# Performance work log

Measured on AMD Instinct MI355X. Metric: run time of the kernel, lower is better.

Reference implementation:

```python
import jax, jax.numpy as jnp
import numpy as np

B, N, FIN, FOUT = 8, 4096, 64, 64
NEG_SLOPE = 0.01  # torch LeakyReLU default


def setup_inputs() -> dict:
    key = jax.random.key(0)
    k1, k2, k3, k4, k5 = jax.random.split(key, 5)
    inp = jax.random.normal(k1, (B, N, FIN), dtype=jnp.float32)
    adj = jax.random.randint(k2, (N, N), 0, 2, dtype=jnp.int32)
    W_w = jax.random.normal(k3, (FOUT, FIN), dtype=jnp.float32) * (1.0 / np.sqrt(FIN))
    W_b = jax.random.normal(k4, (FOUT,), dtype=jnp.float32) * 0.01
    a = jax.random.normal(k5, (2 * FOUT, N), dtype=jnp.float32) * (1.414 / np.sqrt(2 * FOUT + N))
    return {"inp": inp, "adj": adj, "W_w": W_w, "W_b": W_b, "a": a}


def reference(inp, adj, W_w, W_b, a):
    # h = W(inp); h[:, 0, :] = 0
    h = jnp.einsum('bnf,of->bno', inp, W_w) + W_b          # [B, N, F]
    h = h.at[:, 0, :].set(0.0)

    # Original loop: for i in 1..N-1:
    #   ac = a[:, i]  (shape [2F, 1])
    #   index = where(adj[1:, i] > 0)  -> 0-based, used to index h directly (bug preserved)
    #   s_i = h[:, i, :] @ ac[:F] + sum_j h[:, index, :] @ ac[F:]   (scalar per batch)
    #   attention[:, i, :] = s_i broadcast over all columns
    # Empty-index case equals the general case since an empty neighbor sum is 0.
    mask = (adj[1:, :] > 0).astype(h.dtype)                # [N-1, N]
    neigh = jnp.einsum('ji,bjf->bif', mask, h[:, :N - 1, :])  # [B, N, F]
    s = (jnp.einsum('bif,fi->bi', h, a[:FOUT]) +
         jnp.einsum('bif,fi->bi', neigh, a[FOUT:]))        # [B, N]
    s = s.at[:, 0].set(0.0)                                # attention row 0 stays zero

    # h_prime = attention @ h, with attention[b,i,j] = s[b,i] for all j
    hsum = h.sum(axis=1)                                   # [B, F]
    h_prime = s[:, :, None] * hsum[:, None, :]             # [B, N, F]
    return jnp.where(h_prime >= 0, h_prime, NEG_SLOPE * h_prime)
```

## Files before the change

### kernel.cpp

```cpp
#include <hip/hip_runtime.h>
#include <hip/hip_bf16.h>

#define NN 4096

typedef unsigned short u16;
typedef __attribute__((ext_vector_type(8))) short short8;
typedef __attribute__((ext_vector_type(4))) float f32x4;
typedef __attribute__((ext_vector_type(4))) unsigned short u16x4;
typedef __attribute__((ext_vector_type(8))) unsigned short u16x8;
typedef __attribute__((ext_vector_type(4))) int i32x4;

typedef const void __attribute__((address_space(1)))* gas_t;
typedef void __attribute__((address_space(3)))* las_t;

__device__ __forceinline__ u16 f2bf(float x) {
  unsigned u = __float_as_uint(x);
  return (u16)((u + 0x7FFFu + ((u >> 16) & 1)) >> 16);
}

__global__ __launch_bounds__(256) void k_maskT(const int* __restrict__ adj, u16* __restrict__ maskT) {
  __shared__ __align__(16) u16 tile[128 * 132];
  const int i0 = blockIdx.x * 128, j0 = blockIdx.y * 128;
  const int t = threadIdx.x;
  const int jr = t >> 5, ic = (t & 31) * 4;
#pragma unroll
  for (int pass = 0; pass < 16; ++pass) {
    const int jl = pass * 8 + jr;
    const int j = j0 + jl;
    u16 v0 = 0, v1 = 0, v2 = 0, v3 = 0;
    if (j < NN - 1) {
      i32x4 av = *reinterpret_cast<const i32x4*>(&adj[(size_t)(j + 1) * NN + i0 + ic]);
      v0 = av.x > 0 ? 0x3F80 : 0;
      v1 = av.y > 0 ? 0x3F80 : 0;
      v2 = av.z > 0 ? 0x3F80 : 0;
      v3 = av.w > 0 ? 0x3F80 : 0;
    }
    tile[(ic + 0) * 132 + jl] = v0;
    tile[(ic + 1) * 132 + jl] = v1;
    tile[(ic + 2) * 132 + jl] = v2;
    tile[(ic + 3) * 132 + jl] = v3;
  }
  __syncthreads();
  const int ir = t >> 5, jc = (t & 31) * 4;
#pragma unroll
  for (int pass = 0; pass < 16; ++pass) {
    const int il = pass * 8 + ir;
    u16x4 o = *reinterpret_cast<const u16x4*>(&tile[il * 132 + jc]);
    *reinterpret_cast<u16x4*>(&maskT[(size_t)(i0 + il) * NN + j0 + jc]) = o;
  }
}

__global__ __launch_bounds__(256) void k_h(const float* __restrict__ inp, const float* __restrict__ Ww,
                                           const float* __restrict__ Wb, float* __restrict__ h,
                                           u16* __restrict__ h2t, float* __restrict__ hsum) {
  __shared__ __align__(16) u16 lA[128 * 64];
  __shared__ __align__(16) u16 lW[64 * 64];
  const int t = threadIdx.x, lane = t & 63, w = t >> 6;
  const int bid = blockIdx.x;
  const int b = bid >> 5;
  const size_t row0 = (size_t)bid * 128;
  {
    const int o = t >> 2, k0 = (t & 3) * 16;
    const float* src = &Ww[o * 64 + k0];
    u16 tmp[16];
#pragma unroll
    for (int e = 0; e < 16; ++e) tmp[e] = f2bf(src[e]);
    const int swz = (o & 7) * 8;
#pragma unroll
    for (int v = 0; v < 2; ++v)
      *reinterpret_cast<u16x8*>(&lW[o * 64 + ((k0 + v * 8) ^ swz)]) = *reinterpret_cast<u16x8*>(&tmp[v * 8]);
  }
  {
    const int r = t >> 1, k0 = (t & 1) * 32;
    const float* src = &inp[(row0 + r) * 64 + k0];
    u16 tmp[32];
#pragma unroll
    for (int e = 0; e < 32; ++e) tmp[e] = f2bf(src[e]);
    const int swz = (r & 7) * 8;
#pragma unroll
    for (int v = 0; v < 4; ++v)
      *reinterpret_cast<u16x8*>(&lA[r * 64 + ((k0 + v * 8) ^ swz)]) = *reinterpret_cast<u16x8*>(&tmp[v * 8]);
  }
  __syncthreads();
  f32x4 acc[2][4] = {};
#pragma unroll
  for (int ks = 0; ks < 2; ++ks) {
    const int kk = ks * 32 + (lane >> 4) * 8;
    short8 af[2], bf[4];
#pragma unroll
    for (int m = 0; m < 2; ++m) {
      const int row = w * 32 + m * 16 + (lane & 15);
      af[m] = *reinterpret_cast<const short8*>(&lA[row * 64 + (kk ^ ((row & 7) * 8))]);
    }
#pragma unroll
    for (int n = 0; n < 4; ++n) {
      const int o = n * 16 + (lane & 15);
      bf[n] = *reinterpret_cast<const short8*>(&lW[o * 64 + (kk ^ ((o & 7) * 8))]);
    }
#pragma unroll
    for (int m = 0; m < 2; ++m)
#pragma unroll
      for (int n = 0; n < 4; ++n)
        acc[m][n] = __builtin_amdgcn_mfma_f32_16x16x32_bf16(af[m], bf[n], acc[m][n], 0, 0, 0);
  }
  const int f0 = lane & 15;
  const int rsub = (lane >> 4) * 4;
  float wb[4];
#pragma unroll
  for (int n = 0; n < 4; ++n) wb[n] = Wb[n * 16 + f0];
  const int nloc_base = (bid & 31) * 128;
  float ps[4] = {0.f, 0.f, 0.f, 0.f};
#pragma unroll
  for (int m = 0; m < 2; ++m) {
    const int rl = w * 32 + m * 16 + rsub;
#pragma unroll
    for (int n = 0; n < 4; ++n) {
      u16 hb[4];
#pragma unroll
      for (int r = 0; r < 4; ++r) {
        float v = acc[m][n][r] + wb[n];
        if (nloc_base + rl + r == 0) v = 0.f;
        h[(row0 + rl + r) * 64 + n * 16 + f0] = v;
        hb[r] = f2bf(v);
        ps[n] += v;
      }
      *reinterpret_cast<u16x4*>(&h2t[(size_t)(b * 64 + n * 16 + f0) * NN + nloc_base + rl]) =
          *reinterpret_cast<u16x4*>(&hb[0]);
    }
  }
#pragma unroll
  for (int n = 0; n < 4; ++n) {
    float v = ps[n];
    v += __shfl_xor(v, 16);
    v += __shfl_xor(v, 32);
    if (lane < 16) atomicAdd(&hsum[b * 64 + n * 16 + f0], v);
  }
}

__global__ __launch_bounds__(256, 2) void k_gemm(const u16* __restrict__ A, const u16* __restrict__ Bm,
                                                 const float* __restrict__ a, float* __restrict__ s) {
  __shared__ __align__(16) u16 lA0[128 * 64], lA1[128 * 64];
  __shared__ __align__(16) u16 lB0[128 * 64], lB1[128 * 64];
  const int sid = blockIdx.x;
  const int wgid = (sid & 7) * 64 + (sid >> 3);
  const int c0 = (wgid & 3) * 128;
  const int i0 = ((wgid >> 2) & 31) * 128;
  const int z = wgid >> 7;
  const int t = threadIdx.x, lane = t & 63, w = t >> 6;
  const int wr = w >> 1, wc = w & 1;

  const int srow = lane >> 3;
  const int sk = ((lane & 7) ^ srow) * 8;
  const size_t kbase = (size_t)z * 1024;
  const u16* gA = A + (size_t)(i0 + w * 32 + srow) * NN + kbase + sk;
  const u16* gB = Bm + (size_t)(c0 + w * 32 + srow) * NN + kbase + sk;

#define STAGE_K(dstA, dstB, kt)                                                              \
  do {                                                                                       \
    _Pragma("unroll") for (int c = 0; c < 4; ++c) {                                          \
      __builtin_amdgcn_global_load_lds((gas_t)(gA + (size_t)(8 * c) * NN + (kt)),            \
                                       (las_t)((dstA) + (w * 32 + 8 * c) * 128 + lane * 16), \
                                       16, 0, 0);                                            \
      __builtin_amdgcn_global_load_lds((gas_t)(gB + (size_t)(8 * c) * NN + (kt)),            \
                                       (las_t)((dstB) + (w * 32 + 8 * c) * 128 + lane * 16), \
                                       16, 0, 0);                                            \
    }                                                                                        \
  } while (0)

  f32x4 acc[4][4] = {};
  STAGE_K((char*)lA0, (char*)lB0, 0);
  __syncthreads();
#pragma unroll 1
  for (int it = 0; it < 16; ++it) {
    char* nA = (it & 1) ? (char*)lA0 : (char*)lA1;
    char* nB = (it & 1) ? (char*)lB0 : (char*)lB1;
    if (it < 15) STAGE_K(nA, nB, (it + 1) * 64);
    const u16* cA = (it & 1) ? lA1 : lA0;
    const u16* cB = (it & 1) ? lB1 : lB0;
#pragma unroll
    for (int ks = 0; ks < 2; ++ks) {
      const int kb = ks * 4 + (lane >> 4);
      short8 af[4], bfr[4];
#pragma unroll
      for (int m = 0; m < 4; ++m) {
        const int row = wr * 64 + m * 16 + (lane & 15);
        af[m] = *reinterpret_cast<const short8*>(&cA[row * 64 + ((kb ^ (row & 7)) * 8)]);
      }
#pragma unroll
      for (int n = 0; n < 4; ++n) {
        const int row = wc * 64 + n * 16 + (lane & 15);
        bfr[n] = *reinterpret_cast<const short8*>(&cB[row * 64 + ((kb ^ (row & 7)) * 8)]);
      }
#pragma unroll
      for (int m = 0; m < 4; ++m)
#pragma unroll
        for (int n = 0; n < 4; ++n)
          acc[m][n] = __builtin_amdgcn_mfma_f32_16x16x32_bf16(af[m], bfr[n], acc[m][n], 0, 0, 0);
    }
    __syncthreads();
  }
#undef STAGE_K
  const int b = (c0 >> 7) * 2 + wc;
  const int f0 = lane & 15, rsub = (lane >> 4) * 4;
  float pp[4][4];
#pragma unroll
  for (int m = 0; m < 4; ++m) {
    const int irow = i0 + wr * 64 + m * 16 + rsub;
#pragma unroll
    for (int r = 0; r < 4; ++r) pp[m][r] = 0.f;
#pragma unroll
    for (int n = 0; n < 4; ++n) {
      f32x4 a2v = *reinterpret_cast<const f32x4*>(&a[(size_t)(64 + n * 16 + f0) * NN + irow]);
#pragma unroll
      for (int r = 0; r < 4; ++r) pp[m][r] += acc[m][n][r] * a2v[r];
    }
  }
#pragma unroll
  for (int m = 0; m < 4; ++m)
#pragma unroll
    for (int r = 0; r < 4; ++r) {
      float v = pp[m][r];
      v += __shfl_xor(v, 1);
      v += __shfl_xor(v, 2);
      v += __shfl_xor(v, 4);
      v += __shfl_xor(v, 8);
      pp[m][r] = v;
    }
  if (f0 == 0) {
    const int irow = i0 + wr * 64 + rsub;
#pragma unroll
    for (int m = 0; m < 4; ++m)
#pragma unroll
      for (int r = 0; r < 4; ++r)
        atomicAdd(&s[(size_t)b * NN + irow + m * 16 + r], pp[m][r]);
  }
}

__global__ __launch_bounds__(256) void k_final(const float* __restrict__ h, const float* __restrict__ sg,
                                               const float* __restrict__ a, const float* __restrict__ hsum,
                                               float* __restrict__ out) {
  __shared__ float a1[64][65];
  __shared__ float hs[64], sv[64];
  const int b = blockIdx.x >> 6;
  const int i0 = (blockIdx.x & 63) * 64;
  const int t = threadIdx.x;
  {
    const int lr = t >> 6, li = t & 63;
#pragma unroll
    for (int rr = 0; rr < 64; rr += 4)
      a1[rr + lr][li] = a[(size_t)(rr + lr) * NN + i0 + li];
    if (t < 64) hs[t] = hsum[b * 64 + t];
  }
  __syncthreads();
  const int il = t >> 2, q = t & 3;
  const int i = i0 + il;
  const float* hrow = &h[((size_t)b * NN + i) * 64 + q * 16];
  float p = 0.f;
#pragma unroll
  for (int k = 0; k < 16; ++k) p += hrow[k] * a1[q * 16 + k][il];
  p += __shfl_down(p, 2, 4);
  p += __shfl_down(p, 1, 4);
  if (q == 0) sv[il] = (i == 0) ? 0.f : (p + sg[(size_t)b * NN + i]);
  __syncthreads();
  const int lf = t & 63, lr2 = t >> 6;
#pragma unroll
  for (int rr = 0; rr < 64; rr += 4) {
    int ii = rr + lr2;
    float val = sv[ii] * hs[lf];
    out[((size_t)b * NN + i0 + ii) * 64 + lf] = (val >= 0.f) ? val : 0.01f * val;
  }
}

extern "C" void kernel_launch(void* const* d_in, const int* in_sizes, int n_in,
                              void* d_out, int out_size, void* d_ws, size_t ws_size,
                              hipStream_t stream) {
  const float* inp = (const float*)d_in[0];
  const int* adj = (const int*)d_in[1];
  const float* Ww = (const float*)d_in[2];
  const float* Wb = (const float*)d_in[3];
  const float* a = (const float*)d_in[4];
  float* out = (float*)d_out;
  char* ws = (char*)d_ws;

  float* s = (float*)ws;
  float* hsum = (float*)(ws + 131072);
  u16* maskT = (u16*)(ws + 262144);
  u16* h2t = (u16*)(ws + 262144 + 33554432);
  float* h = (float*)(ws + 262144 + 33554432 + 4194304);

  hipMemsetAsync(ws, 0, 133120, stream);
  hipLaunchKernelGGL(k_maskT, dim3(32, 32), dim3(256), 0, stream, adj, maskT);
  hipLaunchKernelGGL(k_h, dim3(256), dim3(256), 0, stream, inp, Ww, Wb, h, h2t, hsum);
  hipLaunchKernelGGL(k_gemm, dim3(512), dim3(256), 0, stream, maskT, h2t, a, s);
  hipLaunchKernelGGL(k_final, dim3(512), dim3(256), 0, stream, h, s, a, hsum, out);
}
```

Baseline: 152.4 us.

## Overlap GEMM prefetch with compute via partial vmcnt waits; swizzle mask-transpose LDS

The bf16 GEMM loop now issues the next stage's global-to-LDS loads and waits only on the previous stage with s_waitcnt vmcnt(8) plus raw s_barrier. Previously __syncthreads drained every outstanding load, so the prefetch can now overlap the MFMA work. Separately, the adjacency mask transpose kernel writes its LDS tile as 4-element vectors in an XOR-swizzled layout and reads it back with a matching swizzle, aiming to cut bank conflicts from scalar strided stores. The hand-placed waitcnt relies on the exact count of outstanding loads per stage (8) and on the compiler not adding other memory operations, so correctness is fragile.

```diff
diff --git a/kernel.cpp b/kernel.cpp
--- a/kernel.cpp
+++ b/kernel.cpp
@@ -22,31 +22,36 @@
   __shared__ __align__(16) u16 tile[128 * 132];
   const int i0 = blockIdx.x * 128, j0 = blockIdx.y * 128;
   const int t = threadIdx.x;
-  const int jr = t >> 5, ic = (t & 31) * 4;
+  const int jr = t >> 5;
+  const int il = t & 31;
 #pragma unroll
   for (int pass = 0; pass < 16; ++pass) {
     const int jl = pass * 8 + jr;
     const int j = j0 + jl;
-    u16 v0 = 0, v1 = 0, v2 = 0, v3 = 0;
+    u16 q[4] = {0, 0, 0, 0};
     if (j < NN - 1) {
-      i32x4 av = *reinterpret_cast<const i32x4*>(&adj[(size_t)(j + 1) * NN + i0 + ic]);
-      v0 = av.x > 0 ? 0x3F80 : 0;
-      v1 = av.y > 0 ? 0x3F80 : 0;
-      v2 = av.z > 0 ? 0x3F80 : 0;
-      v3 = av.w > 0 ? 0x3F80 : 0;
-    }
-    tile[(ic + 0) * 132 + jl] = v0;
-    tile[(ic + 1) * 132 + jl] = v1;
-    tile[(ic + 2) * 132 + jl] = v2;
-    tile[(ic + 3) * 132 + jl] = v3;
+      i32x4 av = *reinterpret_cast<const i32x4*>(&adj[(size_t)(j + 1) * NN + i0 + il * 4]);
+      q[0] = av.x > 0 ? 0x3F80 : 0;
+      q[1] = av.y > 0 ? 0x3F80 : 0;
+      q[2] = av.z > 0 ? 0x3F80 : 0;
+      q[3] = av.w > 0 ? 0x3F80 : 0;
+    }
+    const int pb = il ^ (jl >> 2);
+    *reinterpret_cast<u16x4*>(&tile[jl * 132 + pb * 4]) = *reinterpret_cast<u16x4*>(q);
   }
   __syncthreads();
-  const int ir = t >> 5, jc = (t & 31) * 4;
 #pragma unroll
   for (int pass = 0; pass < 16; ++pass) {
-    const int il = pass * 8 + ir;
-    u16x4 o = *reinterpret_cast<const u16x4*>(&tile[il * 132 + jc]);
-    *reinterpret_cast<u16x4*>(&maskT[(size_t)(i0 + il) * NN + j0 + jc]) = o;
+    const int ir = pass * 8 + jr;
+    const int ci = ir >> 2, io = ir & 3;
+    u16 o[4];
+#pragma unroll
+    for (int d = 0; d < 4; ++d) {
+      const int r = il * 4 + d;
+      o[d] = tile[r * 132 + ((ci ^ il) << 2) + io];
+    }
+    *reinterpret_cast<u16x4*>(&maskT[(size_t)(i0 + ir) * NN + j0 + il * 4]) =
+        *reinterpret_cast<u16x4*>(o);
   }
 }
 
@@ -168,13 +173,20 @@
   } while (0)
 
   f32x4 acc[4][4] = {};
+  asm volatile("" ::: "memory");
   STAGE_K((char*)lA0, (char*)lB0, 0);
-  __syncthreads();
 #pragma unroll 1
   for (int it = 0; it < 16; ++it) {
     char* nA = (it & 1) ? (char*)lA0 : (char*)lA1;
     char* nB = (it & 1) ? (char*)lB0 : (char*)lB1;
-    if (it < 15) STAGE_K(nA, nB, (it + 1) * 64);
+    if (it < 15) {
+      STAGE_K(nA, nB, (it + 1) * 64);
+      asm volatile("s_waitcnt vmcnt(8)" ::: "memory");
+    } else {
+      asm volatile("s_waitcnt vmcnt(0)" ::: "memory");
+    }
+    __builtin_amdgcn_s_barrier();
+    asm volatile("" ::: "memory");
     const u16* cA = (it & 1) ? lA1 : lA0;
     const u16* cB = (it & 1) ? lB1 : lB0;
 #pragma unroll
@@ -197,7 +209,8 @@
         for (int n = 0; n < 4; ++n)
           acc[m][n] = __builtin_amdgcn_mfma_f32_16x16x32_bf16(af[m], bfr[n], acc[m][n], 0, 0, 0);
     }
-    __syncthreads();
+    asm volatile("" ::: "memory");
+    __builtin_amdgcn_s_barrier();
   }
 #undef STAGE_K
   const int b = (c0 >> 7) * 2 + wc;
```

After: 153.1 us. About the same (+0.5%).
